# Kernel tuning notes

Measured on AMD Instinct MI355X. Metric: run time of the kernel, lower is better.

The kernel has to match this reference:

```python
import jax, jax.numpy as jnp
import numpy as np
from jax import lax

V, C_IN, P = 40000, 4, 32
D, H, W = 4, 200, 200          # grid_size (200,200,4)=[X,Y,Z] -> dense (D,H,W)
HID, OUT = 64, 256
B = 2
EPS = 1e-5


def setup_inputs() -> dict:
    key = jax.random.key(0)
    ks = jax.random.split(key, 12)
    voxels = jax.random.normal(ks[0], (V, C_IN, P), dtype=jnp.float32)
    # unique occupied cells so scatter-set is order independent (faithful to last-write loop)
    rng = np.random.default_rng(0)
    lin = rng.choice(D * H * W, size=V, replace=False)
    z = lin // (H * W)
    rem = lin % (H * W)
    y = rem // W
    x = rem % W
    indices = jnp.asarray(np.stack([x, y, z], axis=1), dtype=jnp.int32)  # [V,3] = (x,y,z)
    s = 0.05
    w1 = jax.random.normal(ks[1], (HID, C_IN, 3, 3, 3), jnp.float32) * s
    b1 = jnp.zeros((HID,), jnp.float32)
    g1 = jnp.ones((HID,), jnp.float32)
    be1 = jnp.zeros((HID,), jnp.float32)
    w2 = jax.random.normal(ks[2], (HID, HID, 3, 3, 3), jnp.float32) * s
    b2 = jnp.zeros((HID,), jnp.float32)
    g2 = jnp.ones((HID,), jnp.float32)
    be2 = jnp.zeros((HID,), jnp.float32)
    wh = jax.random.normal(ks[3], (OUT, HID * D, 1, 1), jnp.float32) * s
    bh = jnp.zeros((OUT,), jnp.float32)
    return dict(voxels=voxels, indices=indices, batch_size=B,
                w1=w1, b1=b1, g1=g1, be1=be1,
                w2=w2, b2=b2, g2=g2, be2=be2, wh=wh, bh=bh)


def _conv3d(x, w, b):
    y = lax.conv_general_dilated(x, w, window_strides=(1, 1, 1), padding='SAME',
                                 dimension_numbers=('NCDHW', 'OIDHW', 'NCDHW'))
    return y + b[None, :, None, None, None]


def _bn_relu(x, g, b):
    # BatchNorm3d in training mode: biased batch stats over (N,D,H,W)
    m = x.mean(axis=(0, 2, 3, 4), keepdims=True)
    v = x.var(axis=(0, 2, 3, 4), keepdims=True)
    y = (x - m) * lax.rsqrt(v + EPS)
    y = g[None, :, None, None, None] * y + b[None, :, None, None, None]
    return jax.nn.relu(y)


def reference(voxels, indices, batch_size, w1, b1, g1, be1, w2, b2, g2, be2, wh, bh):
    # PseudoSparseConv3d: mean over points, scatter into dense grid
    feat = voxels.mean(axis=2)  # [V, C_IN]
    grid = jnp.zeros((D, H, W, C_IN), voxels.dtype)
    grid = grid.at[indices[:, 2], indices[:, 1], indices[:, 0]].set(feat)
    dense = jnp.broadcast_to(jnp.transpose(grid, (3, 0, 1, 2))[None],
                             (batch_size, C_IN, D, H, W))  # same scatter for every batch slot
    x = _bn_relu(_conv3d(dense, w1, b1), g1, be1)          # [B, HID, D, H, W]
    x = _bn_relu(_conv3d(x, w2, b2), g2, be2)              # SparseConv3d block
    # HeightPooling: [B, C, D, H, W] -> [B, C*D, H, W] -> 1x1 conv
    x = x.reshape(batch_size, HID * D, H, W)
    y = lax.conv_general_dilated(x, wh, window_strides=(1, 1), padding='SAME',
                                 dimension_numbers=('NCHW', 'OIHW', 'NCHW'))
    return y + bh[None, :, None, None]
```

## Files before the change

kernel.cpp:

```cpp
#include <hip/hip_runtime.h>


#define VN   40000
#define CIN  4
#define PN   32
#define SP2  40000
#define SP3  160000
#define HID  64
#define OUTC 256
#define EPSF 1e-5f

typedef __attribute__((ext_vector_type(8)))  short short8;
typedef __attribute__((ext_vector_type(16))) float f32x16;

__device__ inline unsigned short f2bf(float f) {
    unsigned u = __builtin_bit_cast(unsigned, f);
    return (unsigned short)((u + 0x7fffu + ((u >> 16) & 1u)) >> 16);
}
__device__ inline float bf2f(unsigned short h) {
    return __builtin_bit_cast(float, ((unsigned)h) << 16);
}
__device__ inline short8 ld8(const unsigned short* p) {
    return __builtin_bit_cast(short8, *reinterpret_cast<const uint4*>(p));
}

__global__ __launch_bounds__(256) void k_zero(uint4* __restrict__ p) {
    p[blockIdx.x * 256 + threadIdx.x] = make_uint4(0, 0, 0, 0);
}

__global__ __launch_bounds__(256) void k_prep(const float* __restrict__ vox,
                                              const int* __restrict__ idx,
                                              const float* __restrict__ W1,
                                              const float* __restrict__ W2,
                                              const float* __restrict__ WH,
                                              unsigned short* __restrict__ G8,
                                              unsigned short* __restrict__ A1,
                                              unsigned short* __restrict__ A2,
                                              unsigned short* __restrict__ AH) {
    int i = blockIdx.x * 256 + threadIdx.x;
    if (i < VN) {
        int v = i;
        const float4* p = reinterpret_cast<const float4*>(vox + (size_t)v * CIN * PN);
        float m[4];
#pragma unroll
        for (int c = 0; c < 4; ++c) {
            float s = 0.f;
#pragma unroll
            for (int q = 0; q < PN / 4; ++q) {
                float4 r = p[c * (PN / 4) + q];
                s += (r.x + r.y) + (r.z + r.w);
            }
            m[c] = s * (1.f / PN);
        }
        int x = idx[v * 3 + 0], y = idx[v * 3 + 1], z = idx[v * 3 + 2];
        size_t sp = (size_t)z * SP2 + y * 200 + x;
        uint2 o;
        o.x = (unsigned)f2bf(m[0]) | ((unsigned)f2bf(m[1]) << 16);
        o.y = (unsigned)f2bf(m[2]) | ((unsigned)f2bf(m[3]) << 16);
        *reinterpret_cast<uint2*>(G8 + sp * 8) = o;
        return;
    }
    int k = i - VN;
    if (k < 14336) {
        int j = k & 7, l = (k >> 3) & 63, mt = (k >> 9) & 1, s = k >> 10;
        int co = mt * 32 + (l & 31);
        int tap = s * 2 + (l >> 5);
        float v = 0.f;
        if (tap < 27 && j < 4) v = W1[(co * 4 + j) * 27 + tap];
        A1[k] = f2bf(v);
    } else if (k < 124928) {
        int k2 = k - 14336;
        int j = k2 & 7, l = (k2 >> 3) & 63, mt = (k2 >> 9) & 1, cib = (k2 >> 10) & 3, tap = k2 >> 12;
        int co = mt * 32 + (l & 31);
        int ci = cib * 16 + (l >> 5) * 8 + j;
        A2[k2] = f2bf(W2[(co * 64 + ci) * 27 + tap]);
    } else if (k < 190464) {
        int k3 = k - 124928;
        int j = k3 & 7, l = (k3 >> 3) & 63, mtg = (k3 >> 9) & 7, cib = k3 >> 12;
        int o = mtg * 32 + (l & 31);
        int kp = cib * 16 + (l >> 5) * 8 + j;
        int hid = kp & 63, d = kp >> 6;
        AH[k3] = f2bf(WH[o * 256 + hid * 4 + d]);
    }
}

__global__ __launch_bounds__(128) void k_conv1m(const unsigned short* __restrict__ G8,
                                                const unsigned short* __restrict__ A1,
                                                const float* __restrict__ B1,
                                                unsigned short* __restrict__ Y1) {
    __shared__ unsigned short win[360 * 8];
    int bh = blockIdx.x / 25, bw = blockIdx.x % 25;
    int h0 = bh * 4, w0 = bw * 8;
    int t = threadIdx.x;
    for (int e = t; e < 360; e += 128) {
        int p6 = e / 60, rr = e % 60;
        int hh = rr / 10, ww = rr % 10;
        int ps = p6 - 1, hg = h0 + hh - 1, wg = w0 + ww - 1;
        uint4 v = make_uint4(0, 0, 0, 0);
        if ((unsigned)ps < 4u && (unsigned)hg < 200u && (unsigned)wg < 200u)
            v = *reinterpret_cast<const uint4*>(G8 + (size_t)(ps * SP2 + hg * 200 + wg) * 8);
        *reinterpret_cast<uint4*>(win + e * 8) = v;
    }
    __syncthreads();
    int wv = t >> 6, l = t & 63;
    int hi = l >> 5, h_off = (l & 31) >> 3, w = l & 7;
    int d0 = wv * 2;
    f32x16 acc[2][2] = {};
#pragma unroll
    for (int s = 0; s < 14; ++s) {
        int tap = s * 2 + hi; if (tap > 26) tap = 26;
        int kd = tap / 9, r9 = tap % 9, kh = r9 / 3, kw = r9 % 3;
        const uint4* ap = reinterpret_cast<const uint4*>(A1) + (s * 2) * 64 + l;
        short8 a0 = __builtin_bit_cast(short8, ap[0]);
        short8 a1 = __builtin_bit_cast(short8, ap[64]);
#pragma unroll
        for (int nt = 0; nt < 2; ++nt) {
            int cell = (d0 + nt + kd) * 60 + (h_off + kh) * 10 + (w + kw);
            short8 bfr = ld8(win + cell * 8);
            acc[0][nt] = __builtin_amdgcn_mfma_f32_32x32x16_bf16(a0, bfr, acc[0][nt], 0, 0, 0);
            acc[1][nt] = __builtin_amdgcn_mfma_f32_32x32x16_bf16(a1, bfr, acc[1][nt], 0, 0, 0);
        }
    }
    const float4* Bv = reinterpret_cast<const float4*>(B1);
#pragma unroll
    for (int mt = 0; mt < 2; ++mt) {
#pragma unroll
        for (int nt = 0; nt < 2; ++nt) {
            int sp = (d0 + nt) * SP2 + (h0 + h_off) * 200 + (w0 + w);
#pragma unroll
            for (int rq = 0; rq < 4; ++rq) {
                int co0 = mt * 32 + rq * 8 + hi * 4;
                float4 bb = Bv[co0 >> 2];
                uint2 o;
                o.x = (unsigned)f2bf(acc[mt][nt][rq * 4 + 0] + bb.x) |
                      ((unsigned)f2bf(acc[mt][nt][rq * 4 + 1] + bb.y) << 16);
                o.y = (unsigned)f2bf(acc[mt][nt][rq * 4 + 2] + bb.z) |
                      ((unsigned)f2bf(acc[mt][nt][rq * 4 + 3] + bb.w) << 16);
                *reinterpret_cast<uint2*>(Y1 + (size_t)sp * 64 + co0) = o;
            }
        }
    }
}

__global__ __launch_bounds__(256, 5) void k_conv2m(const unsigned short* __restrict__ X,
                                                   const unsigned short* __restrict__ A2,
                                                   const float* __restrict__ AB1,
                                                   const float* __restrict__ B2,
                                                   unsigned short* __restrict__ Y2) {
    __shared__ unsigned short win[240 * 64];
    int bh = blockIdx.x / 25, bw = blockIdx.x % 25;
    int h0 = bh * 4, w0 = bw * 8;
    int t = threadIdx.x;
    int s8 = (t & 7) * 8;
    float a8[8], b8[8];
#pragma unroll
    for (int j = 0; j < 8; ++j) { a8[j] = AB1[s8 + j]; b8[j] = AB1[64 + s8 + j]; }
#pragma unroll
    for (int i = 0; i < 8; ++i) {
        int cell = i * 32 + (t >> 3);
        if (cell < 240) {
            int p = cell / 60, rr = cell % 60;
            int hh = rr / 10, ww = rr % 10;
            int hg = h0 + hh - 1, wg = w0 + ww - 1;
            uint4 st = make_uint4(0, 0, 0, 0);
            if ((unsigned)hg < 200u && (unsigned)wg < 200u) {
                uint4 raw = *reinterpret_cast<const uint4*>(X + (size_t)(p * SP2 + hg * 200 + wg) * 64 + s8);
                unsigned r[4] = {raw.x, raw.y, raw.z, raw.w};
                unsigned q[4];
#pragma unroll
                for (int k = 0; k < 4; ++k) {
                    float lo = bf2f((unsigned short)(r[k] & 0xffff));
                    float hv = bf2f((unsigned short)(r[k] >> 16));
                    lo = fmaxf(fmaf(a8[k * 2], lo, b8[k * 2]), 0.f);
                    hv = fmaxf(fmaf(a8[k * 2 + 1], hv, b8[k * 2 + 1]), 0.f);
                    q[k] = (unsigned)f2bf(lo) | ((unsigned)f2bf(hv) << 16);
                }
                st = make_uint4(q[0], q[1], q[2], q[3]);
            }
            int slot = (t & 7) ^ (cell & 7);
            *reinterpret_cast<uint4*>(win + cell * 64 + slot * 8) = st;
        }
    }
    __syncthreads();
    int wv = t >> 6, l = t & 63;
    int hi = l >> 5, hb = (l & 31) >> 3, w = l & 7;
    int d = wv;
    const uint4* A2v = reinterpret_cast<const uint4*>(A2);
    f32x16 acc[2] = {};
    for (int kd = 0; kd < 3; ++kd) {
        int p = d + kd - 1;
        if ((unsigned)p >= 4u) continue;
        int tap0 = kd * 9;
#pragma unroll
        for (int khw = 0; khw < 9; ++khw) {
            int kh = khw / 3, kw = khw % 3;
            int tap = tap0 + khw;
            int cell = p * 60 + (hb + kh) * 10 + (w + kw);
            const uint4* apb = A2v + ((tap * 4) * 2) * 64 + l;
            uint4 Ar[8];
#pragma unroll
            for (int j = 0; j < 8; ++j) Ar[j] = apb[j * 64];
            uint4 Br[4];
#pragma unroll
            for (int cib = 0; cib < 4; ++cib) {
                int kch = cib * 2 + hi;
                Br[cib] = *reinterpret_cast<const uint4*>(win + cell * 64 + ((kch ^ (cell & 7)) << 3));
            }
#pragma unroll
            for (int cib = 0; cib < 4; ++cib) {
                short8 b = __builtin_bit_cast(short8, Br[cib]);
                acc[0] = __builtin_amdgcn_mfma_f32_32x32x16_bf16(
                    __builtin_bit_cast(short8, Ar[cib * 2]), b, acc[0], 0, 0, 0);
                acc[1] = __builtin_amdgcn_mfma_f32_32x32x16_bf16(
                    __builtin_bit_cast(short8, Ar[cib * 2 + 1]), b, acc[1], 0, 0, 0);
            }
        }
    }
    const float4* Bv = reinterpret_cast<const float4*>(B2);
    int sp = d * SP2 + (h0 + hb) * 200 + (w0 + w);
#pragma unroll
    for (int mt = 0; mt < 2; ++mt) {
#pragma unroll
        for (int rq = 0; rq < 4; ++rq) {
            int co0 = mt * 32 + rq * 8 + hi * 4;
            float4 bb = Bv[co0 >> 2];
            uint2 o;
            o.x = (unsigned)f2bf(acc[mt][rq * 4 + 0] + bb.x) |
                  ((unsigned)f2bf(acc[mt][rq * 4 + 1] + bb.y) << 16);
            o.y = (unsigned)f2bf(acc[mt][rq * 4 + 2] + bb.z) |
                  ((unsigned)f2bf(acc[mt][rq * 4 + 3] + bb.w) << 16);
            *reinterpret_cast<uint2*>(Y2 + (size_t)sp * 64 + co0) = o;
        }
    }
}

__global__ __launch_bounds__(256) void k_stats2p(const unsigned short* __restrict__ Y,
                                                 float* __restrict__ P) {
    int bid = blockIdx.x, t = threadIdx.x, wv = t >> 6, l = t & 63;
    int cg = l & 7, rsub = l >> 3;
    float s[8] = {}, q[8] = {};
    int rend = bid * 625 + 625;
    for (int r = bid * 625 + wv * 8 + rsub; r < rend; r += 32) {
        uint4 raw = *reinterpret_cast<const uint4*>(Y + (size_t)r * 64 + cg * 8);
        unsigned rr[4] = {raw.x, raw.y, raw.z, raw.w};
#pragma unroll
        for (int k = 0; k < 4; ++k) {
            float lo = bf2f((unsigned short)(rr[k] & 0xffff));
            float hv = bf2f((unsigned short)(rr[k] >> 16));
            s[2 * k] += lo;     q[2 * k] += lo * lo;
            s[2 * k + 1] += hv; q[2 * k + 1] += hv * hv;
        }
    }
#pragma unroll
    for (int k = 0; k < 8; ++k) {
#pragma unroll
        for (int m = 8; m < 64; m <<= 1) {
            s[k] += __shfl_xor(s[k], m);
            q[k] += __shfl_xor(q[k], m);
        }
    }
    __shared__ float ls[4][128];
    if (l < 8) {
#pragma unroll
        for (int k = 0; k < 8; ++k) {
            ls[wv][cg * 8 + k] = s[k];
            ls[wv][64 + cg * 8 + k] = q[k];
        }
    }
    __syncthreads();
    if (t < 128) P[bid * 128 + t] = ls[0][t] + ls[1][t] + ls[2][t] + ls[3][t];
}

__global__ __launch_bounds__(1024) void k_statsf(const float* __restrict__ P,
                                                 const float* __restrict__ G,
                                                 const float* __restrict__ BE,
                                                 float* __restrict__ AB) {
    __shared__ float red[8][128];
    int t = threadIdx.x, c = t & 127, grp = t >> 7;
    float S = 0.f;
    for (int b = grp; b < 256; b += 8) S += P[(size_t)b * 128 + c];
    red[grp][c] = S;
    __syncthreads();
    if (t < 128) {
        float v = 0.f;
#pragma unroll
        for (int g = 0; g < 8; ++g) v += red[g][t];
        red[0][t] = v;
    }
    __syncthreads();
    if (t < 64) {
        float m = red[0][t] * (1.f / SP3);
        float var = red[0][64 + t] * (1.f / SP3) - m * m;
        float a = G[t] * rsqrtf(var + EPSF);
        AB[t] = a; AB[64 + t] = BE[t] - m * a;
    }
}

__global__ __launch_bounds__(256) void k_headm(const unsigned short* __restrict__ X,
                                               const unsigned short* __restrict__ AH,
                                               const float* __restrict__ AB2,
                                               const float* __restrict__ BH,
                                               float* __restrict__ O, int dup2) {
    __shared__ float sab[128];
    int t = threadIdx.x;
    if (t < 128) sab[t] = AB2[t];
    __syncthreads();
    int wv = t >> 6, l = t & 63, khalf = l >> 5;
    int coh = wv >> 1, colh = wv & 1;
    int sp = blockIdx.x * 64 + colh * 32 + (l & 31);
    f32x16 acc[4] = {};
#pragma unroll
    for (int cib = 0; cib < 16; ++cib) {
        int d = cib >> 2, ch0 = (cib & 3) * 16 + khalf * 8;
        uint4 raw = *(const uint4*)(X + ((size_t)(d * SP2 + sp)) * 64 + ch0);
        unsigned r[4] = {raw.x, raw.y, raw.z, raw.w}, qq[4];
#pragma unroll
        for (int k2 = 0; k2 < 4; ++k2) {
            int c0 = ch0 + k2 * 2;
            float lo = bf2f((unsigned short)(r[k2] & 0xffff));
            float hi = bf2f((unsigned short)(r[k2] >> 16));
            lo = fmaxf(fmaf(sab[c0], lo, sab[64 + c0]), 0.f);
            hi = fmaxf(fmaf(sab[c0 + 1], hi, sab[64 + c0 + 1]), 0.f);
            qq[k2] = (unsigned)f2bf(lo) | ((unsigned)f2bf(hi) << 16);
        }
        short8 bfr = __builtin_bit_cast(short8, make_uint4(qq[0], qq[1], qq[2], qq[3]));
#pragma unroll
        for (int mi = 0; mi < 4; ++mi) {
            const uint4* ap = (const uint4*)AH + (cib * 8 + coh * 4 + mi) * 64 + l;
            short8 afr = __builtin_bit_cast(short8, *ap);
            acc[mi] = __builtin_amdgcn_mfma_f32_32x32x16_bf16(afr, bfr, acc[mi], 0, 0, 0);
        }
    }
#pragma unroll
    for (int mi = 0; mi < 4; ++mi) {
#pragma unroll
        for (int rq = 0; rq < 4; ++rq) {
            int co0 = coh * 128 + mi * 32 + rq * 8 + khalf * 4;
            float4 bb = *(const float4*)(BH + co0);
#pragma unroll
            for (int j = 0; j < 4; ++j) {
                float val = acc[mi][rq * 4 + j] + ((const float*)&bb)[j];
                size_t o = (size_t)(co0 + j) * SP2 + sp;
                O[o] = val;
                if (dup2) O[10240000 + o] = val;
            }
        }
    }
}

__global__ __launch_bounds__(256) void k_dup(float* __restrict__ O) {
    int i = blockIdx.x * 256 + threadIdx.x;
    float4* p = reinterpret_cast<float4*>(O);
    p[OUTC * SP2 / 4 + i] = p[i];
}

extern "C" void kernel_launch(void* const* d_in, const int* in_sizes, int n_in,
                              void* d_out, int out_size, void* d_ws, size_t ws_size,
                              hipStream_t stream) {
    const float* vox = (const float*)d_in[0];
    const int*   idx = (const int*)d_in[1];
    const float* w1  = (const float*)d_in[3];
    const float* b1  = (const float*)d_in[4];
    const float* g1  = (const float*)d_in[5];
    const float* be1 = (const float*)d_in[6];
    const float* w2  = (const float*)d_in[7];
    const float* b2  = (const float*)d_in[8];
    const float* g2  = (const float*)d_in[9];
    const float* be2 = (const float*)d_in[10];
    const float* wh  = (const float*)d_in[11];
    const float* bh  = (const float*)d_in[12];

    float* out = (float*)d_out;
    char* ws = (char*)d_ws;
    unsigned short* grid8  = (unsigned short*)ws;
    float*          ab1    = (float*)(ws + 2560000);
    float*          ab2    = (float*)(ws + 2560512);
    float*          part   = (float*)(ws + 2561024);
    unsigned short* apack1 = (unsigned short*)(ws + 2692096);
    unsigned short* apack2 = (unsigned short*)(ws + 2720768);
    unsigned short* apackh = (unsigned short*)(ws + 2941952);

    bool ws_mode = ws_size >= 44033024u;
    unsigned short* y1b, * y2b;
    if (ws_mode) {
        y1b = (unsigned short*)(ws + 3073024);
        y2b = (unsigned short*)(ws + 23553024);
    } else {
        y1b = (unsigned short*)(out + 10240000);
        y2b = y1b + 10240000;
    }

    k_zero<<<625, 256, 0, stream>>>((uint4*)grid8);
    k_prep<<<901, 256, 0, stream>>>(vox, idx, w1, w2, wh, grid8, apack1, apack2, apackh);
    k_conv1m<<<1250, 128, 0, stream>>>(grid8, apack1, b1, y1b);
    k_stats2p<<<256, 256, 0, stream>>>(y1b, part);
    k_statsf<<<1, 1024, 0, stream>>>(part, g1, be1, ab1);
    k_conv2m<<<1250, 256, 0, stream>>>(y1b, apack2, ab1, b2, y2b);
    k_stats2p<<<256, 256, 0, stream>>>(y2b, part);
    k_statsf<<<1, 1024, 0, stream>>>(part, g2, be2, ab2);
    k_headm<<<625, 256, 0, stream>>>(y2b, apackh, ab2, bh, out, ws_mode ? 1 : 0);
    if (!ws_mode)
        k_dup<<<10000, 256, 0, stream>>>(out);
}
```

Before: 135.9 us.

## Fuse BatchNorm statistics into conv epilogues and drop separate stats passes

Each conv kernel now reduces per-channel sum and sum of squares of its pre-bias fp32 accumulators with wave shuffles and writes per-block partials. The finalize kernel folds the bias back in analytically. This removes two kernels that re-read the full bf16 activation tensors. The conv2 inner loop also loads A fragments per channel block instead of all at once, which may reduce register pressure. Statistics now come from unrounded fp32 values rather than bf16, and the finalize step must sum 1250 partials instead of 256.

```diff
diff --git a/kernel.cpp b/kernel.cpp
--- a/kernel.cpp
+++ b/kernel.cpp
@@ -87,7 +87,8 @@
 __global__ __launch_bounds__(128) void k_conv1m(const unsigned short* __restrict__ G8,
                                                 const unsigned short* __restrict__ A1,
                                                 const float* __restrict__ B1,
-                                                unsigned short* __restrict__ Y1) {
+                                                unsigned short* __restrict__ Y1,
+                                                float* __restrict__ part) {
     __shared__ unsigned short win[360 * 8];
     int bh = blockIdx.x / 25, bw = blockIdx.x % 25;
     int h0 = bh * 4, w0 = bw * 8;
@@ -140,13 +141,40 @@
             }
         }
     }
+    __syncthreads();
+    float* ps = (float*)win;
+#pragma unroll
+    for (int mt = 0; mt < 2; ++mt) {
+#pragma unroll
+        for (int rq = 0; rq < 4; ++rq) {
+#pragma unroll
+            for (int j = 0; j < 4; ++j) {
+                float u = acc[mt][0][rq * 4 + j] + acc[mt][1][rq * 4 + j];
+                float q = acc[mt][0][rq * 4 + j] * acc[mt][0][rq * 4 + j]
+                        + acc[mt][1][rq * 4 + j] * acc[mt][1][rq * 4 + j];
+#pragma unroll
+                for (int m = 1; m < 32; m <<= 1) {
+                    u += __shfl_xor(u, m);
+                    q += __shfl_xor(q, m);
+                }
+                if ((l & 31) == 0) {
+                    int co = mt * 32 + rq * 8 + hi * 4 + j;
+                    ps[wv * 128 + co] = u;
+                    ps[wv * 128 + 64 + co] = q;
+                }
+            }
+        }
+    }
+    __syncthreads();
+    if (t < 128) part[(size_t)blockIdx.x * 128 + t] = ps[t] + ps[128 + t];
 }
 
 __global__ __launch_bounds__(256, 5) void k_conv2m(const unsigned short* __restrict__ X,
                                                    const unsigned short* __restrict__ A2,
                                                    const float* __restrict__ AB1,
                                                    const float* __restrict__ B2,
-                                                   unsigned short* __restrict__ Y2) {
+                                                   unsigned short* __restrict__ Y2,
+                                                   float* __restrict__ part) {
     __shared__ unsigned short win[240 * 64];
     int bh = blockIdx.x / 25, bw = blockIdx.x % 25;
     int h0 = bh * 4, w0 = bw * 8;
@@ -197,22 +225,14 @@
             int tap = tap0 + khw;
             int cell = p * 60 + (hb + kh) * 10 + (w + kw);
             const uint4* apb = A2v + ((tap * 4) * 2) * 64 + l;
-            uint4 Ar[8];
-#pragma unroll
-            for (int j = 0; j < 8; ++j) Ar[j] = apb[j * 64];
-            uint4 Br[4];
 #pragma unroll
             for (int cib = 0; cib < 4; ++cib) {
+                short8 a0 = __builtin_bit_cast(short8, apb[cib * 2 * 64]);
+                short8 a1 = __builtin_bit_cast(short8, apb[(cib * 2 + 1) * 64]);
                 int kch = cib * 2 + hi;
-                Br[cib] = *reinterpret_cast<const uint4*>(win + cell * 64 + ((kch ^ (cell & 7)) << 3));
-            }
-#pragma unroll
-            for (int cib = 0; cib < 4; ++cib) {
-                short8 b = __builtin_bit_cast(short8, Br[cib]);
-                acc[0] = __builtin_amdgcn_mfma_f32_32x32x16_bf16(
-                    __builtin_bit_cast(short8, Ar[cib * 2]), b, acc[0], 0, 0, 0);
-                acc[1] = __builtin_amdgcn_mfma_f32_32x32x16_bf16(
-                    __builtin_bit_cast(short8, Ar[cib * 2 + 1]), b, acc[1], 0, 0, 0);
+                short8 b = ld8(win + cell * 64 + ((kch ^ (cell & 7)) << 3));
+                acc[0] = __builtin_amdgcn_mfma_f32_32x32x16_bf16(a0, b, acc[0], 0, 0, 0);
+                acc[1] = __builtin_amdgcn_mfma_f32_32x32x16_bf16(a1, b, acc[1], 0, 0, 0);
             }
         }
     }
@@ -232,53 +252,44 @@
             *reinterpret_cast<uint2*>(Y2 + (size_t)sp * 64 + co0) = o;
         }
     }
-}
-
-__global__ __launch_bounds__(256) void k_stats2p(const unsigned short* __restrict__ Y,
-                                                 float* __restrict__ P) {
-    int bid = blockIdx.x, t = threadIdx.x, wv = t >> 6, l = t & 63;
-    int cg = l & 7, rsub = l >> 3;
-    float s[8] = {}, q[8] = {};
-    int rend = bid * 625 + 625;
-    for (int r = bid * 625 + wv * 8 + rsub; r < rend; r += 32) {
-        uint4 raw = *reinterpret_cast<const uint4*>(Y + (size_t)r * 64 + cg * 8);
-        unsigned rr[4] = {raw.x, raw.y, raw.z, raw.w};
-#pragma unroll
-        for (int k = 0; k < 4; ++k) {
-            float lo = bf2f((unsigned short)(rr[k] & 0xffff));
-            float hv = bf2f((unsigned short)(rr[k] >> 16));
-            s[2 * k] += lo;     q[2 * k] += lo * lo;
-            s[2 * k + 1] += hv; q[2 * k + 1] += hv * hv;
-        }
-    }
-#pragma unroll
-    for (int k = 0; k < 8; ++k) {
-#pragma unroll
-        for (int m = 8; m < 64; m <<= 1) {
-            s[k] += __shfl_xor(s[k], m);
-            q[k] += __shfl_xor(q[k], m);
-        }
-    }
-    __shared__ float ls[4][128];
-    if (l < 8) {
-#pragma unroll
-        for (int k = 0; k < 8; ++k) {
-            ls[wv][cg * 8 + k] = s[k];
-            ls[wv][64 + cg * 8 + k] = q[k];
-        }
-    }
-    __syncthreads();
-    if (t < 128) P[bid * 128 + t] = ls[0][t] + ls[1][t] + ls[2][t] + ls[3][t];
-}
-
-__global__ __launch_bounds__(1024) void k_statsf(const float* __restrict__ P,
+    __syncthreads();
+    float* ps = (float*)win;
+#pragma unroll
+    for (int mt = 0; mt < 2; ++mt) {
+#pragma unroll
+        for (int rq = 0; rq < 4; ++rq) {
+#pragma unroll
+            for (int j = 0; j < 4; ++j) {
+                float u = acc[mt][rq * 4 + j];
+                float q = u * u;
+#pragma unroll
+                for (int m = 1; m < 32; m <<= 1) {
+                    u += __shfl_xor(u, m);
+                    q += __shfl_xor(q, m);
+                }
+                if ((l & 31) == 0) {
+                    int co = mt * 32 + rq * 8 + hi * 4 + j;
+                    ps[wv * 128 + co] = u;
+                    ps[wv * 128 + 64 + co] = q;
+                }
+            }
+        }
+    }
+    __syncthreads();
+    if (t < 128)
+        part[(size_t)blockIdx.x * 128 + t] =
+            ps[t] + ps[128 + t] + ps[256 + t] + ps[384 + t];
+}
+
+__global__ __launch_bounds__(1024) void k_statsf(const float* __restrict__ P, int nblk,
+                                                 const float* __restrict__ BIAS,
                                                  const float* __restrict__ G,
                                                  const float* __restrict__ BE,
                                                  float* __restrict__ AB) {
     __shared__ float red[8][128];
     int t = threadIdx.x, c = t & 127, grp = t >> 7;
     float S = 0.f;
-    for (int b = grp; b < 256; b += 8) S += P[(size_t)b * 128 + c];
+    for (int b = grp; b < nblk; b += 8) S += P[(size_t)b * 128 + c];
     red[grp][c] = S;
     __syncthreads();
     if (t < 128) {
@@ -289,8 +300,12 @@
     }
     __syncthreads();
     if (t < 64) {
-        float m = red[0][t] * (1.f / SP3);
-        float var = red[0][64 + t] * (1.f / SP3) - m * m;
+        float b = BIAS[t];
+        float Su = red[0][t], Qu = red[0][64 + t];
+        float Sb = Su + 160000.f * b;
+        float Qb = Qu + 2.f * b * Su + 160000.f * b * b;
+        float m = Sb * (1.f / 160000.f);
+        float var = Qb * (1.f / 160000.f) - m * m;
         float a = G[t] * rsqrtf(var + EPSF);
         AB[t] = a; AB[64 + t] = BE[t] - m * a;
     }
@@ -376,15 +391,15 @@
     float*          ab1    = (float*)(ws + 2560000);
     float*          ab2    = (float*)(ws + 2560512);
     float*          part   = (float*)(ws + 2561024);
-    unsigned short* apack1 = (unsigned short*)(ws + 2692096);
-    unsigned short* apack2 = (unsigned short*)(ws + 2720768);
-    unsigned short* apackh = (unsigned short*)(ws + 2941952);
-
-    bool ws_mode = ws_size >= 44033024u;
+    unsigned short* apack1 = (unsigned short*)(ws + 3201024);
+    unsigned short* apack2 = (unsigned short*)(ws + 3229696);
+    unsigned short* apackh = (unsigned short*)(ws + 3450880);
+
+    bool ws_mode = ws_size >= 44541952u;
     unsigned short* y1b, * y2b;
     if (ws_mode) {
-        y1b = (unsigned short*)(ws + 3073024);
-        y2b = (unsigned short*)(ws + 23553024);
+        y1b = (unsigned short*)(ws + 3581952);
+        y2b = (unsigned short*)(ws + 24061952);
     } else {
         y1b = (unsigned short*)(out + 10240000);
         y2b = y1b + 10240000;
@@ -392,12 +407,10 @@
 
     k_zero<<<625, 256, 0, stream>>>((uint4*)grid8);
     k_prep<<<901, 256, 0, stream>>>(vox, idx, w1, w2, wh, grid8, apack1, apack2, apackh);
-    k_conv1m<<<1250, 128, 0, stream>>>(grid8, apack1, b1, y1b);
-    k_stats2p<<<256, 256, 0, stream>>>(y1b, part);
-    k_statsf<<<1, 1024, 0, stream>>>(part, g1, be1, ab1);
-    k_conv2m<<<1250, 256, 0, stream>>>(y1b, apack2, ab1, b2, y2b);
-    k_stats2p<<<256, 256, 0, stream>>>(y2b, part);
-    k_statsf<<<1, 1024, 0, stream>>>(part, g2, be2, ab2);
+    k_conv1m<<<1250, 128, 0, stream>>>(grid8, apack1, b1, y1b, part);
+    k_statsf<<<1, 1024, 0, stream>>>(part, 1250, b1, g1, be1, ab1);
+    k_conv2m<<<1250, 256, 0, stream>>>(y1b, apack2, ab1, b2, y2b, part);
+    k_statsf<<<1, 1024, 0, stream>>>(part, 1250, b2, g2, be2, ab2);
     k_headm<<<625, 256, 0, stream>>>(y2b, apackh, ab2, bh, out, ws_mode ? 1 : 0);
     if (!ws_mode)
         k_dup<<<10000, 256, 0, stream>>>(out);
```

Result: slower. 201.2 us (+48.0%).
